# Kernel optimization log

Measured on AMD Instinct MI355X. Metric: run time of the kernel, lower is better.

The kernel has to match this reference:

```python
import jax, jax.numpy as jnp
import numpy as np

B, G = 16, 16384
C, S, L = 8, 8, 4


def setup_inputs() -> dict:
    key = jax.random.key(0)
    kx, kI = jax.random.split(key)
    # valuation vectors in [0,1): probabilities of ground atoms
    x = jax.random.uniform(kx, (B, G), dtype=jnp.float32)
    # clause index tensor: I[c, g, s, l] is an index into the G ground atoms
    I = jax.random.randint(kI, (C, G, S, L), 0, G, dtype=jnp.int64)
    return {"x": x, "I": I}


def reference(x, I):
    """Differentiable forward-chaining clause-body evaluation (sum variant).

    For each clause c, target atom g, substitution s:
      body[c, b, g, s] = prod_l x[b, I[c, g, s, l]]
    then sum over substitutions s. Output shape (C, B, G).
    """
    gathered = x[:, I]                      # (B, C, G, S, L) gather along G
    body = jnp.prod(gathered, axis=-1)      # (B, C, G, S) conjunction over body atoms
    out = jnp.sum(body, axis=-1)            # (B, C, G) sum over substitutions
    return jnp.moveaxis(out, 0, 1)          # (C, B, G) to match torch stack over clauses
```

## Files before the change

kernel.cpp:

```cpp
#include <hip/hip_runtime.h>

namespace {
constexpr int kB = 16;
constexpr int kG = 16384;
constexpr int kC = 8;
constexpr int kS = 8;
constexpr int kLogG = 14;
constexpr int kChunks = 64;
constexpr int kCGPerChunk = (kC * kG) / kChunks;
constexpr int kThreads = 1024;
constexpr int kGroups = kThreads / 4;
constexpr int kIters = kCGPerChunk / kGroups;
}

typedef _Float16 h4 __attribute__((ext_vector_type(4)));

template <int CTRL>
__device__ __forceinline__ float qperm(float x) {
    int r = __builtin_amdgcn_update_dpp(0, __builtin_bit_cast(int, x),
                                        CTRL, 0xF, 0xF, true);
    return __builtin_bit_cast(float, r);
}

__global__ __launch_bounds__(kThreads) void clause_eval_lds(
        const float* __restrict__ x, const int* __restrict__ idx,
        float* __restrict__ out) {
    extern __shared__ h4 xs[];

    const int bid = blockIdx.x;
    const int xcd = bid & 7;
    const int slot = bid >> 3;
    const int part = slot & 3;
    const int chunk = (slot >> 2) * 8 + xcd;

    const int t = threadIdx.x;
    const int sq = t & 3;
    const int gid = t >> 2;
    const int cgbase = chunk * kCGPerChunk;
    const int4* ibase = (const int4*)idx;

    const size_t ib0 = (size_t)(cgbase + gid) * kS;
    int4 ca0 = ibase[ib0 + sq];
    int4 ca1 = ibase[ib0 + sq + 4];
    int4 na0 = ibase[ib0 + (size_t)kGroups * kS + sq];
    int4 na1 = ibase[ib0 + (size_t)kGroups * kS + sq + 4];

#pragma unroll
    for (int pass = 0; pass < kG / (kThreads * 4); ++pass) {
        const int g0 = (pass * kThreads + t) * 4;
        const float4 r0 = *(const float4*)(x + (part * 4 + 0) * kG + g0);
        const float4 r1 = *(const float4*)(x + (part * 4 + 1) * kG + g0);
        const float4 r2 = *(const float4*)(x + (part * 4 + 2) * kG + g0);
        const float4 r3 = *(const float4*)(x + (part * 4 + 3) * kG + g0);
        union { h4 h[2]; float4 f; } p0, p1;
        p0.h[0] = h4{(_Float16)r0.x, (_Float16)r1.x, (_Float16)r2.x, (_Float16)r3.x};
        p0.h[1] = h4{(_Float16)r0.y, (_Float16)r1.y, (_Float16)r2.y, (_Float16)r3.y};
        p1.h[0] = h4{(_Float16)r0.z, (_Float16)r1.z, (_Float16)r2.z, (_Float16)r3.z};
        p1.h[1] = h4{(_Float16)r0.w, (_Float16)r1.w, (_Float16)r2.w, (_Float16)r3.w};
        float4* dst = (float4*)(xs + g0);
        dst[0] = p0.f;
        dst[1] = p1.f;
    }
    __syncthreads();

    const int c = chunk >> 3;
    float* ob = out + c * (kB * kG) + (part * 4 + sq) * kG
                    + ((chunk & 7) * kCGPerChunk + gid);

#pragma unroll
    for (int j = 0; j < kIters; ++j) {
        const int4 b0 = ca0, b1 = ca1;
        ca0 = na0; ca1 = na1;
        if (j + 2 < kIters) {
            const size_t ibn = ib0 + (size_t)(j + 2) * kGroups * kS;
            na0 = ibase[ibn + sq];
            na1 = ibase[ibn + sq + 4];
        }

        h4 q = xs[b0.x] * xs[b0.y] * xs[b0.z] * xs[b0.w]
             + xs[b1.x] * xs[b1.y] * xs[b1.z] * xs[b1.w];
        float4 v = make_float4((float)q[0], (float)q[1], (float)q[2], (float)q[3]);

        const bool hi2 = (sq & 2) != 0;
        float c0 = (hi2 ? v.z : v.x) + qperm<0x4E>(hi2 ? v.x : v.z);
        float c1 = (hi2 ? v.w : v.y) + qperm<0x4E>(hi2 ? v.y : v.w);
        const bool odd = (sq & 1) != 0;
        float r = (odd ? c1 : c0) + qperm<0xB1>(odd ? c0 : c1);

        ob[j * kGroups] = r;
    }
}

extern "C" void kernel_launch(void* const* d_in, const int* in_sizes, int n_in,
                              void* d_out, int out_size, void* d_ws, size_t ws_size,
                              hipStream_t stream) {
    const float* x = (const float*)d_in[0];
    const int* I = (const int*)d_in[1];
    float* out = (float*)d_out;

    const int grid = kChunks * 4;
    const size_t lds = (size_t)kG * sizeof(h4);
    clause_eval_lds<<<grid, kThreads, lds, stream>>>(x, I, out);
}
```

Measured before the change: 13.20 us.

## Assign contiguous targets per thread, prefetch all indices, vectorize nontemporal output stores

Each group of four threads now handles a contiguous run of kIters target atoms instead of a strided set. All index loads are issued up front, before the LDS fill, rather than through a rolling two-deep prefetch. Results are buffered in registers and written as two float4 nontemporal stores per thread, replacing eight scalar strided stores. This trades higher register pressure and a less coalesced index load pattern across threads for fewer, wider stores and index-load latency hidden behind the LDS staging.

Measured after the change: 14.18 us. 1.07x slower.

```diff
diff --git a/kernel.cpp b/kernel.cpp
--- a/kernel.cpp
+++ b/kernel.cpp
@@ -14,6 +14,7 @@
 }
 
 typedef _Float16 h4 __attribute__((ext_vector_type(4)));
+typedef float f4v __attribute__((ext_vector_type(4)));
 
 template <int CTRL>
 __device__ __forceinline__ float qperm(float x) {
@@ -36,14 +37,16 @@
     const int t = threadIdx.x;
     const int sq = t & 3;
     const int gid = t >> 2;
-    const int cgbase = chunk * kCGPerChunk;
+    const int cg0 = chunk * kCGPerChunk + gid * kIters;
     const int4* ibase = (const int4*)idx;
 
-    const size_t ib0 = (size_t)(cgbase + gid) * kS;
-    int4 ca0 = ibase[ib0 + sq];
-    int4 ca1 = ibase[ib0 + sq + 4];
-    int4 na0 = ibase[ib0 + (size_t)kGroups * kS + sq];
-    int4 na1 = ibase[ib0 + (size_t)kGroups * kS + sq + 4];
+    int4 ia[kIters], ib[kIters];
+    const size_t ib0 = (size_t)cg0 * kS;
+#pragma unroll
+    for (int j = 0; j < kIters; ++j) {
+        ia[j] = ibase[ib0 + (size_t)j * kS + sq];
+        ib[j] = ibase[ib0 + (size_t)j * kS + sq + 4];
+    }
 
 #pragma unroll
     for (int pass = 0; pass < kG / (kThreads * 4); ++pass) {
@@ -63,19 +66,10 @@
     }
     __syncthreads();
 
-    const int c = chunk >> 3;
-    float* ob = out + c * (kB * kG) + (part * 4 + sq) * kG
-                    + ((chunk & 7) * kCGPerChunk + gid);
-
+    float rbuf[kIters];
 #pragma unroll
     for (int j = 0; j < kIters; ++j) {
-        const int4 b0 = ca0, b1 = ca1;
-        ca0 = na0; ca1 = na1;
-        if (j + 2 < kIters) {
-            const size_t ibn = ib0 + (size_t)(j + 2) * kGroups * kS;
-            na0 = ibase[ibn + sq];
-            na1 = ibase[ibn + sq + 4];
-        }
+        const int4 b0 = ia[j], b1 = ib[j];
 
         h4 q = xs[b0.x] * xs[b0.y] * xs[b0.z] * xs[b0.w]
              + xs[b1.x] * xs[b1.y] * xs[b1.z] * xs[b1.w];
@@ -85,10 +79,16 @@
         float c0 = (hi2 ? v.z : v.x) + qperm<0x4E>(hi2 ? v.x : v.z);
         float c1 = (hi2 ? v.w : v.y) + qperm<0x4E>(hi2 ? v.y : v.w);
         const bool odd = (sq & 1) != 0;
-        float r = (odd ? c1 : c0) + qperm<0xB1>(odd ? c0 : c1);
+        rbuf[j] = (odd ? c1 : c0) + qperm<0xB1>(odd ? c0 : c1);
+    }
 
-        ob[j * kGroups] = r;
-    }
+    const int c = chunk >> 3;
+    const int gbase = (chunk & 7) * kCGPerChunk + gid * kIters;
+    float* ob = out + c * (kB * kG) + (part * 4 + sq) * kG + gbase;
+    f4v o0 = {rbuf[0], rbuf[1], rbuf[2], rbuf[3]};
+    f4v o1 = {rbuf[4], rbuf[5], rbuf[6], rbuf[7]};
+    __builtin_nontemporal_store(o0, (f4v*)ob);
+    __builtin_nontemporal_store(o1, (f4v*)(ob + 4));
 }
 
 extern "C" void kernel_launch(void* const* d_in, const int* in_sizes, int n_in,
```

## Prepack x to fp16 in workspace and stream into LDS via direct global-to-LDS loads

Applied to the files above, without the earlier changes.

Adds a small pre-kernel that converts x into packed fp16x4 per atom in a workspace buffer. The main kernel then fills LDS with global_load_lds DMA instead of loading, converting and storing through registers. It also deepens index prefetch to four iterations and issues those loads before the LDS fill. The cost is an extra kernel launch plus a global round trip for the packed x, and the packing is redone on every call. The original single-kernel path is kept as a fallback when the workspace is too small.

New measurement: 18.11 us. +37.2%, slower.

```diff
diff --git a/kernel.cpp b/kernel.cpp
--- a/kernel.cpp
+++ b/kernel.cpp
@@ -22,8 +22,20 @@
     return __builtin_bit_cast(float, r);
 }
 
+__global__ void build_xh(const float* __restrict__ x, h4* __restrict__ xh) {
+    const int g = blockIdx.x * blockDim.x + threadIdx.x;
+    if (g >= kG) return;
+#pragma unroll
+    for (int p = 0; p < 4; ++p) {
+        h4 v;
+#pragma unroll
+        for (int j = 0; j < 4; ++j) v[j] = (_Float16)x[(p * 4 + j) * kG + g];
+        xh[p * kG + g] = v;
+    }
+}
+
 __global__ __launch_bounds__(kThreads) void clause_eval_lds(
-        const float* __restrict__ x, const int* __restrict__ idx,
+        const h4* __restrict__ xh, const int* __restrict__ idx,
         float* __restrict__ out) {
     extern __shared__ h4 xs[];
 
@@ -33,6 +45,70 @@
     const int part = slot & 3;
     const int chunk = (slot >> 2) * 8 + xcd;
 
+    const int t = threadIdx.x;
+    const int sq = t & 3;
+    const int gid = t >> 2;
+    const int cgbase = chunk * kCGPerChunk;
+    const int4* ibase = (const int4*)idx;
+
+    const size_t ib0 = (size_t)(cgbase + gid) * kS;
+    int4 pa[4], pb[4];
+#pragma unroll
+    for (int j = 0; j < 4; ++j) {
+        pa[j] = ibase[ib0 + (size_t)j * kGroups * kS + sq];
+        pb[j] = ibase[ib0 + (size_t)j * kGroups * kS + sq + 4];
+    }
+
+    {
+        const int wave = t >> 6, lane = t & 63;
+        const char* gsrc = (const char*)(xh + (size_t)part * kG);
+#pragma unroll
+        for (int i = 0; i < 8; ++i) {
+            const int off = wave * 8192 + i * 1024;
+            __builtin_amdgcn_global_load_lds(
+                (const __attribute__((address_space(1))) void*)(gsrc + off + lane * 16),
+                (__attribute__((address_space(3))) void*)((char*)xs + off),
+                16, 0, 0);
+        }
+    }
+    __syncthreads();
+
+    const int c = chunk >> 3;
+    float* ob = out + c * (kB * kG) + (part * 4 + sq) * kG
+                    + ((chunk & 7) * kCGPerChunk + gid);
+
+#pragma unroll
+    for (int j = 0; j < kIters; ++j) {
+        const int4 b0 = pa[j & 3], b1 = pb[j & 3];
+        if (j + 4 < kIters) {
+            const size_t ibn = ib0 + (size_t)(j + 4) * kGroups * kS;
+            pa[j & 3] = ibase[ibn + sq];
+            pb[j & 3] = ibase[ibn + sq + 4];
+        }
+
+        h4 q = xs[b0.x] * xs[b0.y] * xs[b0.z] * xs[b0.w]
+             + xs[b1.x] * xs[b1.y] * xs[b1.z] * xs[b1.w];
+        float4 v = make_float4((float)q[0], (float)q[1], (float)q[2], (float)q[3]);
+
+        const bool hi2 = (sq & 2) != 0;
+        float c0 = (hi2 ? v.z : v.x) + qperm<0x4E>(hi2 ? v.x : v.z);
+        float c1 = (hi2 ? v.w : v.y) + qperm<0x4E>(hi2 ? v.y : v.w);
+        const bool odd = (sq & 1) != 0;
+        float r = (odd ? c1 : c0) + qperm<0xB1>(odd ? c0 : c1);
+
+        ob[j * kGroups] = r;
+    }
+}
+
+__global__ __launch_bounds__(kThreads) void clause_eval_fused(
+        const float* __restrict__ x, const int* __restrict__ idx,
+        float* __restrict__ out) {
+    extern __shared__ h4 xs[];
+    const int bid = blockIdx.x;
+    const int xcd = bid & 7;
+    const int slot = bid >> 3;
+    const int part = slot & 3;
+    const int chunk = (slot >> 2) * 8 + xcd;
     const int t = threadIdx.x;
     const int sq = t & 3;
     const int gid = t >> 2;
@@ -66,7 +142,6 @@
     const int c = chunk >> 3;
     float* ob = out + c * (kB * kG) + (part * 4 + sq) * kG
                     + ((chunk & 7) * kCGPerChunk + gid);
-
 #pragma unroll
     for (int j = 0; j < kIters; ++j) {
         const int4 b0 = ca0, b1 = ca1;
@@ -76,17 +151,14 @@
             na0 = ibase[ibn + sq];
             na1 = ibase[ibn + sq + 4];
         }
-
         h4 q = xs[b0.x] * xs[b0.y] * xs[b0.z] * xs[b0.w]
              + xs[b1.x] * xs[b1.y] * xs[b1.z] * xs[b1.w];
         float4 v = make_float4((float)q[0], (float)q[1], (float)q[2], (float)q[3]);
-
         const bool hi2 = (sq & 2) != 0;
         float c0 = (hi2 ? v.z : v.x) + qperm<0x4E>(hi2 ? v.x : v.z);
         float c1 = (hi2 ? v.w : v.y) + qperm<0x4E>(hi2 ? v.y : v.w);
         const bool odd = (sq & 1) != 0;
         float r = (odd ? c1 : c0) + qperm<0xB1>(odd ? c0 : c1);
-
         ob[j * kGroups] = r;
     }
 }
@@ -100,5 +172,13 @@
 
     const int grid = kChunks * 4;
     const size_t lds = (size_t)kG * sizeof(h4);
-    clause_eval_lds<<<grid, kThreads, lds, stream>>>(x, I, out);
+    const size_t xh_bytes = (size_t)4 * kG * sizeof(h4);
+
+    if (ws_size >= xh_bytes) {
+        h4* xh = (h4*)d_ws;
+        build_xh<<<kG / 256, 256, 0, stream>>>(x, xh);
+        clause_eval_lds<<<grid, kThreads, lds, stream>>>(xh, I, out);
+    } else {
+        clause_eval_fused<<<grid, kThreads, lds, stream>>>(x, I, out);
+    }
 }
```
